# Kernel optimization log

Measured on AMD Instinct MI355X. Metric: run time of the kernel, lower is better.

## Reference

```python
import jax, jax.numpy as jnp
import numpy as np

H = 16  # n_heads
EPS = 1e-12  # torch F.normalize eps


def setup_inputs() -> dict:
    key = jax.random.key(0)
    ks = jax.random.split(key, 7)
    dim = 1024
    b, n = 8, 4096
    s = 1.0 / np.sqrt(dim)
    return {
        "x": jax.random.normal(ks[0], (b, n, dim), dtype=jnp.float32),
        "Wq": jax.random.normal(ks[1], (dim, dim), dtype=jnp.float32) * s,
        "Wk": jax.random.normal(ks[2], (dim, dim), dtype=jnp.float32) * s,
        "Wv": jax.random.normal(ks[3], (dim, dim), dtype=jnp.float32) * s,
        "scale": jnp.ones((H, 1, 1), dtype=jnp.float32),
        "Wo": jax.random.normal(ks[4], (dim, dim), dtype=jnp.float32) * s,
        "bo": jnp.zeros((dim,), dtype=jnp.float32),
    }


def _l2norm(t):
    # F.normalize(t, dim=-1, p=2): t / max(||t||_2, eps)
    nrm = jnp.sqrt(jnp.sum(t * t, axis=-1, keepdims=True))
    return t / jnp.maximum(nrm, EPS)


def reference(x, Wq, Wk, Wv, scale, Wo, bo):
    b, n, c = x.shape
    d = c // H

    def proj_t(W):
        # Linear (x @ W.T) -> [b, n, h, d] -> transposed layout [b, h, d, n]
        return (x @ W.T).reshape(b, n, H, d).transpose(0, 2, 3, 1)

    q = _l2norm(proj_t(Wq))  # [b, h, d, n], L2-normalized over tokens
    k = _l2norm(proj_t(Wk))
    v = proj_t(Wv)

    # cross-covariance attention over channel dim: [b, h, d, d]
    attn = jnp.einsum('bhdn,bhen->bhde', k, q) * scale
    attn = jax.nn.softmax(attn, axis=-1)
    out = jnp.einsum('bhde,bhen->bhdn', attn, v)  # [b, h, d, n]

    # faithful to torch: raw view of contiguous [b, h, d, n] into [b, n, c]
    out = out.reshape(b, n, c)
    return out @ Wo.T + bo
```

## Files before the change

### kernel.cpp

```cpp
#include <hip/hip_runtime.h>
#include <stdint.h>


typedef unsigned short u16;
typedef __attribute__((ext_vector_type(8))) short bf16x8;
typedef __attribute__((ext_vector_type(8))) u16 u16x8;
typedef __attribute__((ext_vector_type(4))) u16 u16x4;
typedef __attribute__((ext_vector_type(4))) float f32x4;

__device__ __forceinline__ float bf2f(u16 u) {
  union { unsigned int i; float f; } x;
  x.i = ((unsigned int)u) << 16;
  return x.f;
}
__device__ __forceinline__ u16 f2bf(float f) {
  union { float f; unsigned int i; } x;
  x.f = f;
  unsigned int u = x.i;
  u = u + 0x7fffu + ((u >> 16) & 1u);
  return (u16)(u >> 16);
}

__device__ __forceinline__ void gload16(const u16* g, u16* l) {
  __builtin_amdgcn_global_load_lds(
      (const __attribute__((address_space(1))) void*)g,
      (__attribute__((address_space(3))) void*)l, 16, 0, 0);
}

__global__ __launch_bounds__(256) void cast_kernel(
    const float4* __restrict__ x, const float4* __restrict__ wq,
    const float4* __restrict__ wk, const float4* __restrict__ wv,
    const float4* __restrict__ wo, u16x4* __restrict__ xbf,
    u16x4* __restrict__ wbf) {
  long i = (long)blockIdx.x * 256 + threadIdx.x;
  float4 v = x[i];
  u16x4 o;
  o[0] = f2bf(v.x); o[1] = f2bf(v.y); o[2] = f2bf(v.z); o[3] = f2bf(v.w);
  xbf[i] = o;
  if (i < 1048576) {
    int sel = (int)(i >> 18);
    const float4* s = (sel == 0) ? wq : (sel == 1) ? wk : (sel == 2) ? wv : wo;
    float4 w = s[i & 262143];
    u16x4 ow;
    ow[0] = f2bf(w.x); ow[1] = f2bf(w.y); ow[2] = f2bf(w.z); ow[3] = f2bf(w.w);
    wbf[i] = ow;
  }
}


#define STG(Lb, G, r0, kt)                                                   \
  gload16((G) + (long)((r0) + rl) * 1024 + (kt) * 64 + slswz,                \
          (Lb) + (r0) * 64 + tid * 8)

#define LDB(Bb)                                                              \
  _Pragma("unroll") for (int jj = 0; jj < 4; ++jj)                           \
  _Pragma("unroll") for (int ks = 0; ks < 2; ++ks) {                         \
    const int idx = (wc * 64 + jj * 16 + fm) * 64 + ks * 32 + fk;            \
    bfr[jj][ks] = *(const bf16x8*)((Bb) + (idx ^ swz));                      \
  }

#define LDA(Ab, qr)                                                          \
  _Pragma("unroll") for (int i = 0; i < 4; ++i)                              \
  _Pragma("unroll") for (int ks = 0; ks < 2; ++ks) {                         \
    const int idx = (wr * 128 + (qr)*64 + i * 16 + fm) * 64 + ks * 32 + fk;  \
    afr[i][ks] = *(const bf16x8*)((Ab) + (idx ^ swz));                       \
  }

#define MM(qr, qc)                                                           \
  {                                                                          \
    __builtin_amdgcn_s_setprio(1);                                           \
    _Pragma("unroll") for (int ks = 0; ks < 2; ++ks)                         \
    _Pragma("unroll") for (int i = 0; i < 4; ++i)                            \
    _Pragma("unroll") for (int jj = 0; jj < 2; ++jj)                         \
        acc[(qr)*4 + i][(qc)*2 + jj] =                                       \
            __builtin_amdgcn_mfma_f32_16x16x32_bf16(                         \
                afr[i][ks], bfr[(qc)*2 + jj][ks],                            \
                acc[(qr)*4 + i][(qc)*2 + jj], 0, 0, 0);                      \
    __builtin_amdgcn_s_setprio(0);                                           \
  }

#define LGKM0                                        \
  do {                                               \
    asm volatile("s_waitcnt lgkmcnt(0)" ::: "memory"); \
    __builtin_amdgcn_sched_barrier(0);               \
  } while (0)
#define VM6 asm volatile("s_waitcnt vmcnt(6)" ::: "memory")
#define VM0 asm volatile("s_waitcnt vmcnt(0)" ::: "memory")
#define VMNONE (void)0
#define BAR __builtin_amdgcn_s_barrier()

#define TILE(Ab, Bb, Aoth, kt, S1, S2, VMW)                                  \
  {                                                                          \
          \
    LDB(Bb);                                                                 \
    LDA(Ab, 0);                                                              \
    if (S1) { STG(Aoth, Ag, 128, (kt) + 1); STG(Aoth, Ag, 192, (kt) + 1); }  \
    BAR;                                                                     \
    MM(0, 0);                                                                \
    LGKM0;                                                                   \
    BAR;                                                                     \
                   \
    if (S2) { STG(Bb, Bg, 0, (kt) + 2); STG(Bb, Bg, 64, (kt) + 2); }         \
    BAR;                                                                     \
    MM(0, 1);                                                                \
    BAR;                                                                     \
                                      \
    LDA(Ab, 1);                                                              \
    if (S2) { STG(Bb, Bg, 128, (kt) + 2); STG(Bb, Bg, 192, (kt) + 2); }      \
    BAR;                                                                     \
    MM(1, 0);                                                                \
    LGKM0;                                                                   \
    BAR;                                                                     \
                                                   \
    if (S2) { STG(Ab, Ag, 0, (kt) + 2); STG(Ab, Ag, 64, (kt) + 2); }         \
    BAR;                                                                     \
    MM(1, 1);                                                                \
    VMW;                                                                     \
    BAR;                                                                     \
  }

template <int MODE>
__global__ __launch_bounds__(512, 2) void gemm256(const u16* __restrict__ A,
                                                  const u16* __restrict__ B,
                                                  void* __restrict__ C,
                                                  const float* __restrict__ bias) {
  __shared__ u16 As0[16384];
  __shared__ u16 As1[16384];
  __shared__ u16 Bs0[16384];
  __shared__ u16 Bs1[16384];
  const int tid = threadIdx.x;
  const int lane = tid & 63;
  const int wave = tid >> 6;
  const int wr = wave >> 2;
  const int wc = wave & 3;
  const int m0 = blockIdx.y * 256;
  const int n0 = blockIdx.x * 256;

  long aoff, boff, coff;
  if (MODE == 0) {
    int w = blockIdx.z >> 3;
    int b = blockIdx.z & 7;
    aoff = (long)w * 1048576;
    boff = (long)b * 4194304;
    coff = (long)blockIdx.z * 4194304;
  } else {
    aoff = (long)blockIdx.z * 4194304;
    boff = 0;
    coff = (long)blockIdx.z * 4194304;
  }
  const u16* Ag = A + aoff + (long)m0 * 1024;
  const u16* Bg = B + boff + (long)n0 * 1024;

  const int rl = tid >> 3;
  const int slswz = ((tid & 7) ^ (rl & 7)) * 8;
  const int fm = lane & 15;
  const int fk = (lane >> 4) << 3;
  const int swz = (fm & 7) << 3;

  f32x4 acc[8][4];
  const f32x4 z4 = {0.f, 0.f, 0.f, 0.f};
#pragma unroll
  for (int i = 0; i < 8; i++)
#pragma unroll
    for (int j = 0; j < 4; j++) acc[i][j] = z4;

  bf16x8 afr[4][2], bfr[4][2];

  STG(Bs0, Bg, 0, 0);   STG(Bs0, Bg, 64, 0);
  STG(Bs0, Bg, 128, 0); STG(Bs0, Bg, 192, 0);
  STG(As0, Ag, 0, 0);   STG(As0, Ag, 64, 0);
  STG(As0, Ag, 128, 0); STG(As0, Ag, 192, 0);
  STG(Bs1, Bg, 0, 1);   STG(Bs1, Bg, 64, 1);
  STG(Bs1, Bg, 128, 1); STG(Bs1, Bg, 192, 1);
  STG(As1, Ag, 0, 1);   STG(As1, Ag, 64, 1);
  VM6;
  BAR;

#pragma unroll 1
  for (int it = 0; it < 7; ++it) {
    TILE(As0, Bs0, As1, 2 * it, true, true, VM6);
    TILE(As1, Bs1, As0, 2 * it + 1, true, true, VM6);
  }
  TILE(As0, Bs0, As1, 14, true, false, VM0);
  TILE(As1, Bs1, As0, 15, false, false, VMNONE);

  const int rq = (lane >> 4) * 4;
  const int mBase = m0 + wr * 128;
  const int nBase = n0 + wc * 64;
  if (MODE == 1) {
    float* Cf = (float*)C + coff;
#pragma unroll
    for (int jj = 0; jj < 4; ++jj) {
      float bv = bias[nBase + jj * 16 + fm];
#pragma unroll
      for (int i = 0; i < 8; ++i)
#pragma unroll
        for (int r = 0; r < 4; ++r) {
          int m = mBase + i * 16 + rq + r;
          int n = nBase + jj * 16 + fm;
          Cf[(long)m * 1024 + n] = acc[i][jj][r] + bv;
        }
    }
  } else {
    const int ldc = (MODE == 0) ? 4096 : 1024;
    u16* Cb = (u16*)C + coff;
#pragma unroll
    for (int i = 0; i < 8; ++i)
#pragma unroll
      for (int jj = 0; jj < 4; ++jj)
#pragma unroll
        for (int r = 0; r < 4; ++r) {
          int m = mBase + i * 16 + rq + r;
          int n = nBase + jj * 16 + fm;
          Cb[(long)m * ldc + n] = f2bf(acc[i][jj][r]);
        }
  }
}

__global__ __launch_bounds__(256) void attn_partial(const u16* __restrict__ qk,
                                                    float* __restrict__ attnP,
                                                    float* __restrict__ nsqP) {
  const int bh = blockIdx.x;
  const int b = bh >> 4, h = bh & 15;
  const int tid = threadIdx.x, lane = tid & 63, wave = tid >> 6;
  const int sl = blockIdx.y * 4 + wave;
  const u16* Qg = qk + (long)b * 4194304 + (long)h * 64 * 4096;
  const u16* Kg = Qg + 33554432L;

  const int fm = lane & 15;
  const long kbase = (long)sl * 256 + (lane >> 4) * 8;

  f32x4 acc[4][4];
  const f32x4 z4 = {0.f, 0.f, 0.f, 0.f};
#pragma unroll
  for (int i = 0; i < 4; i++)
#pragma unroll
    for (int j = 0; j < 4; j++) acc[i][j] = z4;
  float sk[4] = {0.f, 0.f, 0.f, 0.f}, sq[4] = {0.f, 0.f, 0.f, 0.f};

  for (int kt = 0; kt < 256; kt += 32) {
    bf16x8 ak[4], aq[4];
#pragma unroll
    for (int i = 0; i < 4; i++) {
      ak[i] = *(const bf16x8*)(Kg + (long)(i * 16 + fm) * 4096 + kbase + kt);
      aq[i] = *(const bf16x8*)(Qg + (long)(i * 16 + fm) * 4096 + kbase + kt);
    }
#pragma unroll
    for (int i = 0; i < 4; i++) {
      const u16x8 kv = (u16x8)ak[i], qv = (u16x8)aq[i];
#pragma unroll
      for (int e = 0; e < 8; e++) {
        float fkk = bf2f(kv[e]); sk[i] += fkk * fkk;
        float fq = bf2f(qv[e]);  sq[i] += fq * fq;
      }
    }
#pragma unroll
    for (int i = 0; i < 4; i++)
#pragma unroll
      for (int j = 0; j < 4; j++)
        acc[i][j] = __builtin_amdgcn_mfma_f32_16x16x32_bf16(ak[i], aq[j],
                                                            acc[i][j], 0, 0, 0);
  }

#pragma unroll
  for (int i = 0; i < 4; i++) {
    sk[i] += __shfl_xor(sk[i], 16); sk[i] += __shfl_xor(sk[i], 32);
    sq[i] += __shfl_xor(sq[i], 16); sq[i] += __shfl_xor(sq[i], 32);
  }
  float* np = nsqP + ((long)sl * 128 + bh) * 128;
  if (lane < 16) {
#pragma unroll
    for (int i = 0; i < 4; i++) {
      np[i * 16 + lane] = sk[i];
      np[64 + i * 16 + lane] = sq[i];
    }
  }
  float* sp = attnP + ((long)sl * 128 + bh) * 4096;
  const int rq = (lane >> 4) * 4;
#pragma unroll
  for (int i = 0; i < 4; i++)
#pragma unroll
    for (int j = 0; j < 4; j++)
#pragma unroll
      for (int r = 0; r < 4; r++)
        sp[(i * 16 + rq + r) * 64 + j * 16 + fm] = acc[i][j][r];
}

__global__ __launch_bounds__(128) void attn_finalize(const float* __restrict__ attnP,
                                                     const float* __restrict__ nsqP,
                                                     const float* __restrict__ scale,
                                                     u16* __restrict__ attnb) {
  const int bh = blockIdx.x;
  const int h = bh & 15;
  const int tid = threadIdx.x;
  __shared__ float rn[2][64];
  {
    int which = tid >> 6, row = tid & 63;
    float s = 0.f;
#pragma unroll
    for (int sl = 0; sl < 16; sl++)
      s += nsqP[((long)sl * 128 + bh) * 128 + which * 64 + row];
    rn[which][row] = 1.0f / fmaxf(sqrtf(s), 1e-12f);
  }
  __syncthreads();
  if (tid < 64) {
    const int d = tid;
    float row[64];
#pragma unroll
    for (int e = 0; e < 64; e++) row[e] = 0.f;
    for (int sl = 0; sl < 16; sl++) {
      const float4* p =
          (const float4*)(attnP + ((long)sl * 128 + bh) * 4096 + d * 64);
#pragma unroll
      for (int e4 = 0; e4 < 16; e4++) {
        float4 v = p[e4];
        row[e4 * 4 + 0] += v.x;
        row[e4 * 4 + 1] += v.y;
        row[e4 * 4 + 2] += v.z;
        row[e4 * 4 + 3] += v.w;
      }
    }
    const float rk = rn[0][d] * scale[h];
    float mx = -1e30f;
#pragma unroll
    for (int e = 0; e < 64; e++) {
      row[e] = row[e] * rk * rn[1][e];
      mx = fmaxf(mx, row[e]);
    }
    float sum = 0.f;
#pragma unroll
    for (int e = 0; e < 64; e++) {
      row[e] = __expf(row[e] - mx);
      sum += row[e];
    }
    float inv = 1.0f / sum;
    u16* out = attnb + ((long)bh * 64 + d) * 64;
#pragma unroll
    for (int e = 0; e < 64; e++) out[e] = f2bf(row[e] * inv);
  }
}

__global__ __launch_bounds__(256) void av_mfma(const u16* __restrict__ attnb,
                                               const u16* __restrict__ vt,
                                               u16* __restrict__ outb) {
  const int bh = blockIdx.y;
  const int b = bh >> 4, h = bh & 15;
  const int n0 = blockIdx.x * 256;
  const int tid = threadIdx.x, lane = tid & 63, wave = tid >> 6;
  __shared__ u16 As[64 * 72];
  {
    const u16* src = attnb + (long)bh * 4096 + (tid >> 2) * 64 + (tid & 3) * 16;
    u16x8 v0 = *(const u16x8*)src;
    u16x8 v1 = *(const u16x8*)(src + 8);
    u16* dst = As + (tid >> 2) * 72 + (tid & 3) * 16;
    *(u16x8*)dst = v0;
    *(u16x8*)(dst + 8) = v1;
  }
  __syncthreads();
  const int fm = lane & 15;
  const int fe = (lane >> 4) * 8;
  const u16* Vg = vt + (long)b * 4194304 + h * 64 + fe;

  f32x4 acc[4][4];
  const f32x4 z4 = {0.f, 0.f, 0.f, 0.f};
#pragma unroll
  for (int i = 0; i < 4; i++)
#pragma unroll
    for (int j = 0; j < 4; j++) acc[i][j] = z4;

  bf16x8 af[4][2];
#pragma unroll
  for (int i = 0; i < 4; i++)
#pragma unroll
    for (int ks = 0; ks < 2; ks++)
      af[i][ks] = *(const bf16x8*)&As[(i * 16 + fm) * 72 + fe + ks * 32];

#pragma unroll
  for (int ks = 0; ks < 2; ks++)
#pragma unroll
    for (int j = 0; j < 4; j++) {
      int n = n0 + wave * 64 + j * 16 + fm;
      bf16x8 bf = *(const bf16x8*)(Vg + (long)n * 1024 + ks * 32);
#pragma unroll
      for (int i = 0; i < 4; i++)
        acc[i][j] = __builtin_amdgcn_mfma_f32_16x16x32_bf16(af[i][ks], bf,
                                                            acc[i][j], 0, 0, 0);
    }

  const int rq = (lane >> 4) * 4;
  u16* Ob = outb + ((long)b * 1024 + h * 64) * 4096;
#pragma unroll
  for (int i = 0; i < 4; i++)
#pragma unroll
    for (int j = 0; j < 4; j++)
#pragma unroll
      for (int r = 0; r < 4; r++) {
        int d = i * 16 + rq + r;
        int n = n0 + wave * 64 + j * 16 + fm;
        Ob[(long)d * 4096 + n] = f2bf(acc[i][j][r]);
      }
}

extern "C" void kernel_launch(void* const* d_in, const int* in_sizes, int n_in,
                              void* d_out, int out_size, void* d_ws, size_t ws_size,
                              hipStream_t stream) {
  const float* x = (const float*)d_in[0];
  const float* Wq = (const float*)d_in[1];
  const float* Wk = (const float*)d_in[2];
  const float* Wv = (const float*)d_in[3];
  const float* scale = (const float*)d_in[4];
  const float* Wo = (const float*)d_in[5];
  const float* bo = (const float*)d_in[6];
  float* out = (float*)d_out;

  u16* xbf = (u16*)d_ws;
  u16* wbf = xbf + 33554432;
  u16* qk = wbf + 4194304;
  u16* vt = qk + 67108864;
  float* attnP = (float*)(vt + 33554432);
  float* nsqP = attnP + 8388608;
  u16* attnb = (u16*)(nsqP + 262144);
  u16* outb = qk;

  cast_kernel<<<32768, 256, 0, stream>>>((const float4*)x, (const float4*)Wq,
                                         (const float4*)Wk, (const float4*)Wv,
                                         (const float4*)Wo, (u16x4*)xbf,
                                         (u16x4*)wbf);
  gemm256<0><<<dim3(16, 4, 16), 512, 0, stream>>>(wbf, xbf, (void*)qk, nullptr);
  gemm256<2><<<dim3(4, 16, 8), 512, 0, stream>>>(xbf, wbf + 2 * 1048576,
                                                 (void*)vt, nullptr);
  attn_partial<<<dim3(128, 4), 256, 0, stream>>>(qk, attnP, nsqP);
  attn_finalize<<<128, 128, 0, stream>>>(attnP, nsqP, scale, attnb);
  av_mfma<<<dim3(16, 128), 256, 0, stream>>>(attnb, vt, outb);
  gemm256<1><<<dim3(4, 16, 8), 512, 0, stream>>>(outb, wbf + 3 * 1048576,
                                                 (void*)out, bo);
}
```

Baseline: 624.3 us.

## Restructure GEMM k-loop into per-k-slice phases and parallelize attention finalize

```diff
diff --git a/kernel.cpp b/kernel.cpp
--- a/kernel.cpp
+++ b/kernel.cpp
@@ -52,71 +52,52 @@
   gload16((G) + (long)((r0) + rl) * 1024 + (kt) * 64 + slswz,                \
           (Lb) + (r0) * 64 + tid * 8)
 
-#define LDB(Bb)                                                              \
-  _Pragma("unroll") for (int jj = 0; jj < 4; ++jj)                           \
-  _Pragma("unroll") for (int ks = 0; ks < 2; ++ks) {                         \
-    const int idx = (wc * 64 + jj * 16 + fm) * 64 + ks * 32 + fk;            \
-    bfr[jj][ks] = *(const bf16x8*)((Bb) + (idx ^ swz));                      \
-  }
-
-#define LDA(Ab, qr)                                                          \
-  _Pragma("unroll") for (int i = 0; i < 4; ++i)                              \
-  _Pragma("unroll") for (int ks = 0; ks < 2; ++ks) {                         \
-    const int idx = (wr * 128 + (qr)*64 + i * 16 + fm) * 64 + ks * 32 + fk;  \
-    afr[i][ks] = *(const bf16x8*)((Ab) + (idx ^ swz));                       \
-  }
-
-#define MM(qr, qc)                                                           \
+#define BRD(Bb, ksel)                                                        \
+  _Pragma("unroll") for (int jj = 0; jj < 4; ++jj) {                         \
+    const int idx = (wc * 64 + jj * 16 + fm) * 64 + (ksel)*32 + fk;          \
+    bfr[jj][ksel] = *(const bf16x8*)((Bb) + (idx ^ swz));                    \
+  }
+
+#define ARD(Ab, qr, ksel)                                                    \
+  _Pragma("unroll") for (int i = 0; i < 4; ++i) {                            \
+    const int idx = (wr * 128 + (qr)*64 + i * 16 + fm) * 64 + (ksel)*32 + fk;\
+    aC[i] = *(const bf16x8*)((Ab) + (idx ^ swz));                            \
+  }
+
+#define MM16(qr, ksel)                                                       \
   {                                                                          \
     __builtin_amdgcn_s_setprio(1);                                           \
-    _Pragma("unroll") for (int ks = 0; ks < 2; ++ks)                         \
     _Pragma("unroll") for (int i = 0; i < 4; ++i)                            \
-    _Pragma("unroll") for (int jj = 0; jj < 2; ++jj)                         \
-        acc[(qr)*4 + i][(qc)*2 + jj] =                                       \
-            __builtin_amdgcn_mfma_f32_16x16x32_bf16(                         \
-                afr[i][ks], bfr[(qc)*2 + jj][ks],                            \
-                acc[(qr)*4 + i][(qc)*2 + jj], 0, 0, 0);                      \
+    _Pragma("unroll") for (int j = 0; j < 4; ++j)                            \
+        acc[(qr)*4 + i][j] = __builtin_amdgcn_mfma_f32_16x16x32_bf16(        \
+            aC[i], bfr[j][ksel], acc[(qr)*4 + i][j], 0, 0, 0);               \
     __builtin_amdgcn_s_setprio(0);                                           \
   }
 
-#define LGKM0                                        \
-  do {                                               \
-    asm volatile("s_waitcnt lgkmcnt(0)" ::: "memory"); \
-    __builtin_amdgcn_sched_barrier(0);               \
-  } while (0)
-#define VM6 asm volatile("s_waitcnt vmcnt(6)" ::: "memory")
+#define LGKM0 asm volatile("s_waitcnt lgkmcnt(0)" ::: "memory")
+#define VM4 asm volatile("s_waitcnt vmcnt(4)" ::: "memory")
 #define VM0 asm volatile("s_waitcnt vmcnt(0)" ::: "memory")
 #define VMNONE (void)0
 #define BAR __builtin_amdgcn_s_barrier()
 
-#define TILE(Ab, Bb, Aoth, kt, S1, S2, VMW)                                  \
+#define TILE(Ab, Bb, Aoth, kt, SA, SB, VMW)                                  \
   {                                                                          \
-          \
-    LDB(Bb);                                                                 \
-    LDA(Ab, 0);                                                              \
-    if (S1) { STG(Aoth, Ag, 128, (kt) + 1); STG(Aoth, Ag, 192, (kt) + 1); }  \
-    BAR;                                                                     \
-    MM(0, 0);                                                                \
-    LGKM0;                                                                   \
-    BAR;                                                                     \
-                   \
-    if (S2) { STG(Bb, Bg, 0, (kt) + 2); STG(Bb, Bg, 64, (kt) + 2); }         \
-    BAR;                                                                     \
-    MM(0, 1);                                                                \
-    BAR;                                                                     \
-                                      \
-    LDA(Ab, 1);                                                              \
-    if (S2) { STG(Bb, Bg, 128, (kt) + 2); STG(Bb, Bg, 192, (kt) + 2); }      \
-    BAR;                                                                     \
-    MM(1, 0);                                                                \
-    LGKM0;                                                                   \
-    BAR;                                                                     \
-                                                   \
-    if (S2) { STG(Ab, Ag, 0, (kt) + 2); STG(Ab, Ag, 64, (kt) + 2); }         \
-    BAR;                                                                     \
-    MM(1, 1);                                                                \
-    VMW;                                                                     \
-    BAR;                                                                     \
+                                                                     \
+    BRD(Bb, 0); ARD(Ab, 0, 0);                                               \
+    if (SA) { STG(Aoth, Ag, 128, (kt) + 1); STG(Aoth, Ag, 192, (kt) + 1); }  \
+    MM16(0, 0); LGKM0; BAR;                                                  \
+                                                                     \
+    BRD(Bb, 1); ARD(Ab, 0, 1);                                               \
+    if (SA) { STG(Aoth, Ag, 0, (kt) + 1); STG(Aoth, Ag, 64, (kt) + 1); }     \
+    MM16(0, 1); LGKM0; BAR;                                                  \
+                                                                     \
+    ARD(Ab, 1, 0);                                                           \
+    if (SB) { STG(Bb, Bg, 0, (kt) + 2); STG(Bb, Bg, 64, (kt) + 2); }         \
+    MM16(1, 0); LGKM0; BAR;                                                  \
+                                                                     \
+    ARD(Ab, 1, 1);                                                           \
+    if (SB) { STG(Bb, Bg, 128, (kt) + 2); STG(Bb, Bg, 192, (kt) + 2); }      \
+    MM16(1, 1); LGKM0; VMW; BAR;                                             \
   }
 
 template <int MODE>
@@ -164,22 +145,21 @@
 #pragma unroll
     for (int j = 0; j < 4; j++) acc[i][j] = z4;
 
-  bf16x8 afr[4][2], bfr[4][2];
+  bf16x8 aC[4], bfr[4][2];
 
   STG(Bs0, Bg, 0, 0);   STG(Bs0, Bg, 64, 0);
   STG(Bs0, Bg, 128, 0); STG(Bs0, Bg, 192, 0);
+  STG(As0, Ag, 128, 0); STG(As0, Ag, 192, 0);
   STG(As0, Ag, 0, 0);   STG(As0, Ag, 64, 0);
-  STG(As0, Ag, 128, 0); STG(As0, Ag, 192, 0);
   STG(Bs1, Bg, 0, 1);   STG(Bs1, Bg, 64, 1);
   STG(Bs1, Bg, 128, 1); STG(Bs1, Bg, 192, 1);
-  STG(As1, Ag, 0, 1);   STG(As1, Ag, 64, 1);
-  VM6;
+  VM4;
   BAR;
 
 #pragma unroll 1
   for (int it = 0; it < 7; ++it) {
-    TILE(As0, Bs0, As1, 2 * it, true, true, VM6);
-    TILE(As1, Bs1, As0, 2 * it + 1, true, true, VM6);
+    TILE(As0, Bs0, As1, 2 * it, true, true, VM4);
+    TILE(As1, Bs1, As0, 2 * it + 1, true, true, VM4);
   }
   TILE(As0, Bs0, As1, 14, true, false, VM0);
   TILE(As1, Bs1, As0, 15, false, false, VMNONE);
@@ -286,15 +266,16 @@
         sp[(i * 16 + rq + r) * 64 + j * 16 + fm] = acc[i][j][r];
 }
 
-__global__ __launch_bounds__(128) void attn_finalize(const float* __restrict__ attnP,
+__global__ __launch_bounds__(256) void attn_finalize(const float* __restrict__ attnP,
                                                      const float* __restrict__ nsqP,
                                                      const float* __restrict__ scale,
                                                      u16* __restrict__ attnb) {
   const int bh = blockIdx.x;
+  const int dz = blockIdx.y;
   const int h = bh & 15;
   const int tid = threadIdx.x;
   __shared__ float rn[2][64];
-  {
+  if (tid < 128) {
     int which = tid >> 6, row = tid & 63;
     float s = 0.f;
 #pragma unroll
@@ -303,41 +284,43 @@
     rn[which][row] = 1.0f / fmaxf(sqrtf(s), 1e-12f);
   }
   __syncthreads();
-  if (tid < 64) {
-    const int d = tid;
-    float row[64];
-#pragma unroll
-    for (int e = 0; e < 64; e++) row[e] = 0.f;
-    for (int sl = 0; sl < 16; sl++) {
-      const float4* p =
-          (const float4*)(attnP + ((long)sl * 128 + bh) * 4096 + d * 64);
-#pragma unroll
-      for (int e4 = 0; e4 < 16; e4++) {
-        float4 v = p[e4];
-        row[e4 * 4 + 0] += v.x;
-        row[e4 * 4 + 1] += v.y;
-        row[e4 * 4 + 2] += v.z;
-        row[e4 * 4 + 3] += v.w;
-      }
-    }
-    const float rk = rn[0][d] * scale[h];
-    float mx = -1e30f;
-#pragma unroll
-    for (int e = 0; e < 64; e++) {
-      row[e] = row[e] * rk * rn[1][e];
-      mx = fmaxf(mx, row[e]);
-    }
-    float sum = 0.f;
-#pragma unroll
-    for (int e = 0; e < 64; e++) {
-      row[e] = __expf(row[e] - mx);
-      sum += row[e];
-    }
-    float inv = 1.0f / sum;
-    u16* out = attnb + ((long)bh * 64 + d) * 64;
-#pragma unroll
-    for (int e = 0; e < 64; e++) out[e] = f2bf(row[e] * inv);
-  }
+  const int d = dz * 32 + (tid >> 3);
+  const int q8 = tid & 3 ? (tid & 7) : (tid & 7);
+  float row[8];
+#pragma unroll
+  for (int e = 0; e < 8; e++) row[e] = 0.f;
+  for (int sl = 0; sl < 16; sl++) {
+    const float4* p = (const float4*)(attnP + ((long)sl * 128 + bh) * 4096 +
+                                      d * 64 + (tid & 7) * 8);
+    float4 v0 = p[0], v1 = p[1];
+    row[0] += v0.x; row[1] += v0.y; row[2] += v0.z; row[3] += v0.w;
+    row[4] += v1.x; row[5] += v1.y; row[6] += v1.z; row[7] += v1.w;
+  }
+  const float rk = rn[0][d] * scale[h];
+  float mx = -1e30f;
+#pragma unroll
+  for (int e = 0; e < 8; e++) {
+    row[e] = row[e] * rk * rn[1][(tid & 7) * 8 + e];
+    mx = fmaxf(mx, row[e]);
+  }
+  mx = fmaxf(mx, __shfl_xor(mx, 1));
+  mx = fmaxf(mx, __shfl_xor(mx, 2));
+  mx = fmaxf(mx, __shfl_xor(mx, 4));
+  float sum = 0.f;
+#pragma unroll
+  for (int e = 0; e < 8; e++) {
+    row[e] = __expf(row[e] - mx);
+    sum += row[e];
+  }
+  sum += __shfl_xor(sum, 1);
+  sum += __shfl_xor(sum, 2);
+  sum += __shfl_xor(sum, 4);
+  float inv = 1.0f / sum;
+  u16x8 o;
+#pragma unroll
+  for (int e = 0; e < 8; e++) o[e] = f2bf(row[e] * inv);
+  *(u16x8*)(attnb + (long)bh * 4096 + d * 64 + (tid & 7) * 8) = o;
+  (void)q8;
 }
 
 __global__ __launch_bounds__(256) void av_mfma(const u16* __restrict__ attnb,
@@ -430,7 +413,7 @@
   gemm256<2><<<dim3(4, 16, 8), 512, 0, stream>>>(xbf, wbf + 2 * 1048576,
                                                  (void*)vt, nullptr);
   attn_partial<<<dim3(128, 4), 256, 0, stream>>>(qk, attnP, nsqP);
-  attn_finalize<<<128, 128, 0, stream>>>(attnP, nsqP, scale, attnb);
+  attn_finalize<<<dim3(128, 2), 256, 0, stream>>>(attnP, nsqP, scale, attnb);
   av_mfma<<<dim3(16, 128), 256, 0, stream>>>(attnb, vt, outb);
   gemm256<1><<<dim3(4, 16, 8), 512, 0, stream>>>(outb, wbf + 3 * 1048576,
                                                  (void*)out, bo);
```

Result: faster. 609.2 us (-2.4%).
